# Kernel optimization log

Measured on AMD Instinct MI355X. Metric: run time of the kernel, lower is better.

The kernel has to match this reference:

```python
import jax, jax.numpy as jnp
import numpy as np

N = 100000        # nodes
E = 1600000       # edges
NFEAT = 256
NHID = 64
NCLASS = 40
NHEADS = 4
ALPHA = 0.2       # LeakyReLU negative slope


def setup_inputs() -> dict:
    key = jax.random.key(0)
    ks = jax.random.split(key, 7)
    h = jax.random.normal(ks[0], (N, NFEAT), jnp.float32)
    src = jax.random.randint(ks[1], (E,), 0, N, dtype=jnp.int32)
    dst = jax.random.randint(ks[2], (E,), 0, N, dtype=jnp.int32)
    edge_index = jnp.stack([src, dst])  # (2, E)
    # learned parameters (xavier-ish scale)
    W_heads = jax.random.normal(ks[3], (NHEADS, NFEAT, NHID), jnp.float32) * 0.066
    a_heads = jax.random.normal(ks[4], (NHEADS, 2 * NHID, 1), jnp.float32) * 0.1
    W_out = jax.random.normal(ks[5], (NHEADS * NHID, NCLASS), jnp.float32) * 0.08
    a_out = jax.random.normal(ks[6], (2 * NCLASS, 1), jnp.float32) * 0.1
    return {"h": h, "edge_index": edge_index, "W_heads": W_heads,
            "a_heads": a_heads, "W_out": W_out, "a_out": a_out}


def gat_layer(h, src, dst, W, a, concat):
    """One GraphAttentionLayer: gather -> per-edge score -> segment softmax -> scatter."""
    Wh = h @ W                                   # (n, F_out)
    n = h.shape[0]
    F_out = Wh.shape[1]
    # a_input @ a == Wh_src @ a[:F] + Wh_dst @ a[F:], avoids (E, 2F) concat
    a_src, a_dst = a[:F_out, 0], a[F_out:, 0]
    e = jax.nn.leaky_relu(Wh[src] @ a_src + Wh[dst] @ a_dst, ALPHA)  # (E,)
    # per-destination segment softmax (stabilized; same math as exp/sum)
    m = jax.ops.segment_max(e, dst, num_segments=n)
    exp_e = jnp.exp(e - m[dst])
    denom = jax.ops.segment_sum(exp_e, dst, num_segments=n)
    att = exp_e / denom[dst]                     # (E,)
    # scatter-aggregate weighted source features
    h_prime = jax.ops.segment_sum(att[:, None] * Wh[src], dst, num_segments=n)
    return jax.nn.elu(h_prime) if concat else h_prime


def reference(h, edge_index, W_heads, a_heads, W_out, a_out):
    src, dst = edge_index[0], edge_index[1]
    # multi-head attention layers, concatenated (dropout inactive in eval)
    x = jnp.concatenate(
        [gat_layer(h, src, dst, W_heads[i], a_heads[i], True) for i in range(NHEADS)],
        axis=1)                                  # (N, NHEADS*NHID)
    x = gat_layer(x, src, dst, W_out, a_out, False)  # (N, NCLASS)
    return jax.nn.log_softmax(x, axis=1)
```

## Files before the change

kernel.cpp:

```cpp
#include <hip/hip_runtime.h>


#define ALPHA 0.2f
constexpr int N_ = 100000;
constexpr int E_ = 1600000;
constexpr long OUTEL = (long)N_ * 40;

typedef __bf16 bf16x8 __attribute__((ext_vector_type(8)));
typedef float f32x4 __attribute__((ext_vector_type(4)));

__global__ void k_sent(float* out, long n, float v) {
    long i = blockIdx.x * 256L + threadIdx.x;
    if (i < n) out[i] = v;
}


__global__ void k_zero(int* p, int n) {
    int i = blockIdx.x * 256 + threadIdx.x;
    if (i < n) p[i] = 0;
}

__global__ void k_count(const int* __restrict__ dst, int* __restrict__ deg) {
    int e = blockIdx.x * 256 + threadIdx.x;
    if (e < E_) {
        int d = dst[e];
        if ((unsigned)d < (unsigned)N_) atomicAdd(&deg[d], 1);
    }
}

__global__ void k_partial(const int* __restrict__ deg, int* __restrict__ part) {
    __shared__ int sd[256];
    int b = blockIdx.x, t = threadIdx.x;
    int base = b * 1024;
    int s = 0;
    for (int i = 0; i < 4; i++) {
        int idx = base + t * 4 + i;
        if (idx < N_) s += deg[idx];
    }
    sd[t] = s;
    __syncthreads();
    for (int o = 128; o; o >>= 1) {
        if (t < o) sd[t] += sd[t + o];
        __syncthreads();
    }
    if (t == 0) part[b] = sd[0];
}

__global__ void k_scan_part(int* part, int nchunks, int* rowptr) {
    if (threadIdx.x == 0 && blockIdx.x == 0) {
        int run = 0;
        for (int b = 0; b < nchunks; b++) {
            int v = part[b];
            part[b] = run;
            run += v;
        }
        rowptr[N_] = run;
    }
}

__global__ void k_scan_final(const int* __restrict__ deg, const int* __restrict__ part,
                             int* __restrict__ rowptr, int* __restrict__ cursor) {
    __shared__ int sd[256];
    int b = blockIdx.x, t = threadIdx.x;
    int base = b * 1024;
    int v[4];
    int s = 0;
    for (int i = 0; i < 4; i++) {
        int idx = base + t * 4 + i;
        v[i] = (idx < N_) ? deg[idx] : 0;
        s += v[i];
    }
    sd[t] = s;
    __syncthreads();
    for (int o = 1; o < 256; o <<= 1) {
        int add = (t >= o) ? sd[t - o] : 0;
        __syncthreads();
        sd[t] += add;
        __syncthreads();
    }
    int off0 = part[b] + (sd[t] - s);
    for (int i = 0; i < 4; i++) {
        int idx = base + t * 4 + i;
        if (idx < N_) {
            rowptr[idx] = off0;
            cursor[idx] = off0;
            off0 += v[i];
        }
    }
}

__global__ void k_fill(const int* __restrict__ src, const int* __restrict__ dst,
                       int* __restrict__ cursor, int* __restrict__ csr) {
    int e = blockIdx.x * 256 + threadIdx.x;
    if (e < E_) {
        int d = dst[e];
        if ((unsigned)d < (unsigned)N_) {
            int p = atomicAdd(&cursor[d], 1);
            if ((unsigned)p < (unsigned)E_) csr[p] = src[e];
        }
    }
}


__global__ __launch_bounds__(320) void k_prepB(const float* __restrict__ Whd,
                                               const float* __restrict__ ah,
                                               __bf16* __restrict__ Bh, __bf16* __restrict__ Bl) {
    int k = blockIdx.x;
    int c = threadIdx.x;
    if (c >= 272) return;
    float v = 0.f;
    if (c < 256) {
        v = Whd[(c >> 6) * 16384 + k * 64 + (c & 63)];
    } else if (c < 264) {
        int hh = (c - 256) & 3;
        int isd = (c >= 260) ? 64 : 0;
        const float* wp = Whd + hh * 16384 + k * 64;
        const float* ap = ah + hh * 128 + isd;
        float s = 0.f;
        for (int j = 0; j < 64; j++) s += wp[j] * ap[j];
        v = s;
    }
    __bf16 hi = (__bf16)v;
    __bf16 lo = (__bf16)(v - (float)hi);
    size_t idx = ((size_t)(k >> 5) * 272 + c) * 32 + (k & 31);
    Bh[idx] = hi;
    Bl[idx] = lo;
}


__global__ __launch_bounds__(256) void k_gemm1m(const float* __restrict__ h,
                                                const __bf16* __restrict__ Bh,
                                                const __bf16* __restrict__ Bl,
                                                float* __restrict__ Wh1,
                                                float* __restrict__ s1s,
                                                float* __restrict__ s1d) {
    int t = threadIdx.x;
    int wv = t >> 6, l = t & 63;
    int l15 = l & 15, lg = l >> 4;
    int rowA = blockIdx.x * 64 + wv * 16 + l15;
    bool rok = rowA < N_;
    const float* hp = h + (size_t)rowA * 256 + lg * 8;

    f32x4 acc[17];
#pragma unroll
    for (int i = 0; i < 17; i++) acc[i] = (f32x4){0.f, 0.f, 0.f, 0.f};

    for (int kc = 0; kc < 8; kc++) {
        float va[8] = {0.f, 0.f, 0.f, 0.f, 0.f, 0.f, 0.f, 0.f};
        if (rok) {
            float4 p = *(const float4*)(hp + kc * 32);
            float4 q = *(const float4*)(hp + kc * 32 + 4);
            va[0] = p.x; va[1] = p.y; va[2] = p.z; va[3] = p.w;
            va[4] = q.x; va[5] = q.y; va[6] = q.z; va[7] = q.w;
        }
        bf16x8 ahi, alo;
#pragma unroll
        for (int j = 0; j < 8; j++) {
            __bf16 hi = (__bf16)va[j];
            ahi[j] = hi;
            alo[j] = (__bf16)(va[j] - (float)hi);
        }
        const __bf16* bph = Bh + ((size_t)kc * 272 + l15) * 32 + lg * 8;
        const __bf16* bpl = Bl + ((size_t)kc * 272 + l15) * 32 + lg * 8;
#pragma unroll
        for (int tt = 0; tt < 17; tt++) {
            bf16x8 bh = *(const bf16x8*)(bph + tt * 512);
            bf16x8 bl = *(const bf16x8*)(bpl + tt * 512);
            acc[tt] = __builtin_amdgcn_mfma_f32_16x16x32_bf16(ahi, bh, acc[tt], 0, 0, 0);
            acc[tt] = __builtin_amdgcn_mfma_f32_16x16x32_bf16(alo, bh, acc[tt], 0, 0, 0);
            acc[tt] = __builtin_amdgcn_mfma_f32_16x16x32_bf16(ahi, bl, acc[tt], 0, 0, 0);
        }
    }

    int rowD0 = blockIdx.x * 64 + wv * 16 + lg * 4;
#pragma unroll
    for (int tt = 0; tt < 16; tt++) {
#pragma unroll
        for (int r = 0; r < 4; r++) {
            int orow = rowD0 + r;
            if (orow < N_) Wh1[(size_t)orow * 256 + tt * 16 + l15] = acc[tt][r];
        }
    }
#pragma unroll
    for (int r = 0; r < 4; r++) {
        int orow = rowD0 + r;
        if (orow < N_) {
            if (l15 < 4) s1s[orow * 4 + l15] = acc[16][r];
            else if (l15 < 8) s1d[orow * 4 + (l15 - 4)] = acc[16][r];
        }
    }
}


__global__ __launch_bounds__(256) void k_att1(const int* __restrict__ rowptr, const int* __restrict__ csr,
                                              const float* __restrict__ s1s, const float* __restrict__ s1d,
                                              float* __restrict__ att1) {
    int t = threadIdx.x;
    int wv = t >> 6, l = t & 63;
    int n = blockIdx.x * 4 + wv;
    int base = rowptr[n], deg = rowptr[n + 1] - base;
    int i = l >> 2, hh = l & 3;
    float sdw = s1d[n * 4 + hh];

    float mx = -INFINITY;
    for (int ib = 0; ib < deg; ib += 16) {
        int e = ib + i;
        if (e < deg) {
            int s = csr[base + e];
            float v = s1s[s * 4 + hh] + sdw;
            v = v > 0.f ? v : ALPHA * v;
            mx = fmaxf(mx, v);
        }
    }
    for (int o = 4; o < 64; o <<= 1) mx = fmaxf(mx, __shfl_xor(mx, o));
    float sm = 0.f;
    for (int ib = 0; ib < deg; ib += 16) {
        int e = ib + i;
        if (e < deg) {
            int s = csr[base + e];
            float v = s1s[s * 4 + hh] + sdw;
            v = v > 0.f ? v : ALPHA * v;
            sm += expf(v - mx);
        }
    }
    for (int o = 4; o < 64; o <<= 1) sm += __shfl_xor(sm, o);
    float inv = (deg > 0) ? 1.f / sm : 0.f;
    for (int ib = 0; ib < deg; ib += 16) {
        int e = ib + i;
        if (e < deg) {
            int s = csr[base + e];
            float v = s1s[s * 4 + hh] + sdw;
            v = v > 0.f ? v : ALPHA * v;
            att1[(size_t)(base + e) * 4 + hh] = expf(v - mx) * inv;
        }
    }
}


constexpr int AGG_BLOCKS = 768;
constexpr int NODES_PER_SWEEP = AGG_BLOCKS * 8;

__global__ __launch_bounds__(512) void k_agg1g(const int* __restrict__ rowptr, const int* __restrict__ csr,
                                               const float* __restrict__ att1, const float* __restrict__ Wh1,
                                               const float* __restrict__ Wo, const float* __restrict__ ao,
                                               float* __restrict__ Wh2,
                                               float* __restrict__ s2s, float* __restrict__ s2d) {
    __shared__ float WoS[256 * 40];
    __shared__ float xs[8][256];
    int t = threadIdx.x;
#pragma unroll
    for (int u = 0; u < 5; u++) {
        int idx = (u * 512 + t) * 4;
        *(float4*)(&WoS[idx]) = *(const float4*)(&Wo[idx]);
    }
    __syncthreads();

    int w = t >> 6, lane = t & 63;
    int f = lane << 2;
    int hw = lane >> 4;
    float a1 = (lane < 40) ? ao[lane] : 0.f;
    float a2 = (lane < 40) ? ao[40 + lane] : 0.f;

    for (int n = blockIdx.x * 8 + w; n < N_; n += NODES_PER_SWEEP) {
        int base = rowptr[n], deg = rowptr[n + 1] - base;

        float4 acc = make_float4(0.f, 0.f, 0.f, 0.f);
        int i = 0;
        for (; i + 3 < deg; i += 4) {
            int b0 = base + i;
            int s0 = csr[b0], s1 = csr[b0 + 1], s2 = csr[b0 + 2], s3 = csr[b0 + 3];
            float at0 = att1[(size_t)b0 * 4 + hw];
            float at1 = att1[(size_t)(b0 + 1) * 4 + hw];
            float at2 = att1[(size_t)(b0 + 2) * 4 + hw];
            float at3 = att1[(size_t)(b0 + 3) * 4 + hw];
            float4 v0 = *(const float4*)(Wh1 + (size_t)s0 * 256 + f);
            float4 v1 = *(const float4*)(Wh1 + (size_t)s1 * 256 + f);
            float4 v2 = *(const float4*)(Wh1 + (size_t)s2 * 256 + f);
            float4 v3 = *(const float4*)(Wh1 + (size_t)s3 * 256 + f);
            acc.x += at0 * v0.x + at1 * v1.x + at2 * v2.x + at3 * v3.x;
            acc.y += at0 * v0.y + at1 * v1.y + at2 * v2.y + at3 * v3.y;
            acc.z += at0 * v0.z + at1 * v1.z + at2 * v2.z + at3 * v3.z;
            acc.w += at0 * v0.w + at1 * v1.w + at2 * v2.w + at3 * v3.w;
        }
        for (; i < deg; i++) {
            int s0 = csr[base + i];
            float at0 = att1[(size_t)(base + i) * 4 + hw];
            float4 v0 = *(const float4*)(Wh1 + (size_t)s0 * 256 + f);
            acc.x += at0 * v0.x;
            acc.y += at0 * v0.y;
            acc.z += at0 * v0.z;
            acc.w += at0 * v0.w;
        }
        acc.x = acc.x > 0.f ? acc.x : (expf(acc.x) - 1.f);
        acc.y = acc.y > 0.f ? acc.y : (expf(acc.y) - 1.f);
        acc.z = acc.z > 0.f ? acc.z : (expf(acc.z) - 1.f);
        acc.w = acc.w > 0.f ? acc.w : (expf(acc.w) - 1.f);
        *(float4*)(&xs[w][f]) = acc;

        float o = 0.f;
        if (lane < 40) {
            for (int k = 0; k < 256; k += 4) {
                float4 xk = *(const float4*)(&xs[w][k]);
                o += xk.x * WoS[k * 40 + lane] + xk.y * WoS[(k + 1) * 40 + lane] +
                     xk.z * WoS[(k + 2) * 40 + lane] + xk.w * WoS[(k + 3) * 40 + lane];
            }
            Wh2[(size_t)n * 40 + lane] = o;
        }
        float r1 = o * a1, r2 = o * a2;
        for (int off = 32; off; off >>= 1) {
            r1 += __shfl_xor(r1, off);
            r2 += __shfl_xor(r2, off);
        }
        if (lane == 0) {
            s2s[n] = r1;
            s2d[n] = r2;
        }
    }
}


__global__ __launch_bounds__(256) void k_l2(const int* __restrict__ rowptr, const int* __restrict__ csr,
                                            const float* __restrict__ s2s, const float* __restrict__ s2d,
                                            const float* __restrict__ Wh2, float* __restrict__ out) {
    int t = threadIdx.x;
    int wv = t >> 6, lane = t & 63;
    int n = blockIdx.x * 4 + wv;
    int base = rowptr[n], deg = rowptr[n + 1] - base;
    float sdw = s2d[n];

    float mx = -INFINITY;
    for (int i = lane; i < deg; i += 64) {
        int s = csr[base + i];
        float e = s2s[s] + sdw;
        e = e > 0.f ? e : ALPHA * e;
        mx = fmaxf(mx, e);
    }
    for (int o = 32; o; o >>= 1) mx = fmaxf(mx, __shfl_xor(mx, o));

    float acc0 = 0.f, acc1 = 0.f, sm0 = 0.f, sm1 = 0.f;
    int i = 0;
    for (; i + 1 < deg; i += 2) {
        int s0 = csr[base + i], s1 = csr[base + i + 1];
        float e0 = s2s[s0] + sdw;
        float e1 = s2s[s1] + sdw;
        e0 = e0 > 0.f ? e0 : ALPHA * e0;
        e1 = e1 > 0.f ? e1 : ALPHA * e1;
        float a0 = expf(e0 - mx);
        float a1 = expf(e1 - mx);
        sm0 += a0; sm1 += a1;
        if (lane < 40) {
            acc0 += a0 * Wh2[(size_t)s0 * 40 + lane];
            acc1 += a1 * Wh2[(size_t)s1 * 40 + lane];
        }
    }
    if (i < deg) {
        int s0 = csr[base + i];
        float e0 = s2s[s0] + sdw;
        e0 = e0 > 0.f ? e0 : ALPHA * e0;
        float a0 = expf(e0 - mx);
        sm0 += a0;
        if (lane < 40) acc0 += a0 * Wh2[(size_t)s0 * 40 + lane];
    }
    float inv = (deg > 0) ? 1.f / (sm0 + sm1) : 0.f;
    float acc = (acc0 + acc1) * inv;

    float v = (lane < 40) ? acc : -INFINITY;
    float mv = v;
    for (int o = 32; o; o >>= 1) mv = fmaxf(mv, __shfl_xor(mv, o));
    float ex = (lane < 40) ? expf(acc - mv) : 0.f;
    float se = ex;
    for (int o = 32; o; o >>= 1) se += __shfl_xor(se, o);
    if (lane < 40) out[(size_t)n * 40 + lane] = acc - mv - logf(se);
}


extern "C" void kernel_launch(void* const* d_in, const int* in_sizes, int n_in,
                              void* d_out, int out_size, void* d_ws, size_t ws_size,
                              hipStream_t stream) {
    const float* h   = (const float*)d_in[0];
    const int*   ei  = (const int*)d_in[1];
    const float* Whd = (const float*)d_in[2];
    const float* ah  = (const float*)d_in[3];
    const float* Wo  = (const float*)d_in[4];
    const float* ao  = (const float*)d_in[5];
    float* out = (float*)d_out;

    const int* src = ei;
    const int* dst = ei + E_;
    const int nchunks = (N_ + 1023) / 1024;

    char* ws = (char*)d_ws;
    size_t off = 0;
    auto alloc = [&](size_t bytes) -> char* {
        size_t a = (off + 255) & ~(size_t)255;
        off = a + bytes;
        return ws + a;
    };
    int* rowptr = (int*)alloc((size_t)(N_ + 1) * 4);
    int* cursor = (int*)alloc((size_t)N_ * 4);
    int* deg    = (int*)alloc((size_t)N_ * 4);
    int* part   = (int*)alloc((size_t)(nchunks + 1) * 4);
    int* csr    = (int*)alloc((size_t)E_ * 4);
    float* s1s  = (float*)alloc((size_t)N_ * 4 * 4);
    float* s1d  = (float*)alloc((size_t)N_ * 4 * 4);
    float* Wh2  = (float*)alloc((size_t)N_ * 40 * 4);
    float* s2s  = (float*)alloc((size_t)N_ * 4);
    float* s2d  = (float*)alloc((size_t)N_ * 4);
    __bf16* Bh  = (__bf16*)alloc((size_t)8 * 272 * 32 * 2);
    __bf16* Bl  = (__bf16*)alloc((size_t)8 * 272 * 32 * 2);
    float* att1 = (float*)alloc((size_t)E_ * 4 * 4);
    float* Wh1  = (float*)alloc((size_t)N_ * 256 * 4);
    size_t need = off + 256;

    if (ws_size < need) {
        k_sent<<<(int)((OUTEL + 255) / 256), 256, 0, stream>>>(out, OUTEL, -2.0f);
        return;
    }

    k_prepB<<<256, 320, 0, stream>>>(Whd, ah, Bh, Bl);

    k_zero<<<(N_ + 255) / 256, 256, 0, stream>>>(deg, N_);
    k_count<<<(E_ + 255) / 256, 256, 0, stream>>>(dst, deg);
    k_partial<<<nchunks, 256, 0, stream>>>(deg, part);
    k_scan_part<<<1, 64, 0, stream>>>(part, nchunks, rowptr);
    k_scan_final<<<nchunks, 256, 0, stream>>>(deg, part, rowptr, cursor);
    k_fill<<<(E_ + 255) / 256, 256, 0, stream>>>(src, dst, cursor, csr);

    k_gemm1m<<<(N_ + 63) / 64, 256, 0, stream>>>(h, Bh, Bl, Wh1, s1s, s1d);
    k_att1<<<N_ / 4, 256, 0, stream>>>(rowptr, csr, s1s, s1d, att1);

    k_agg1g<<<AGG_BLOCKS, 512, 0, stream>>>(rowptr, csr, att1, Wh1, Wo, ao, Wh2, s2s, s2d);

    k_l2<<<N_ / 4, 256, 0, stream>>>(rowptr, csr, s2s, s2d, Wh2, out);
}
```

Baseline: 905.9 us.

## Defer softmax normalization, use readlane matvec, and retile layer-2 aggregation

The attention kernel now stores unnormalized exponentials plus a per-node inverse sum, removing its third pass that re-gathered scores and recomputed exp. The aggregation kernel applies the inverse sum after accumulation, replaces the shared-memory staging of the hidden vector with readlane broadcasts for the 256x40 projection, and raises block count and occupancy hints. The layer-2 kernel splits the wave into 8 edge groups by 8 column groups of 5 classes, so edges are processed in parallel instead of serially two at a time. The cost is an extra small buffer, more shuffle reductions, and heavier register use from the unrolled readlane loop.

```diff
diff --git a/kernel.cpp b/kernel.cpp
--- a/kernel.cpp
+++ b/kernel.cpp
@@ -194,7 +194,7 @@
 
 __global__ __launch_bounds__(256) void k_att1(const int* __restrict__ rowptr, const int* __restrict__ csr,
                                               const float* __restrict__ s1s, const float* __restrict__ s1d,
-                                              float* __restrict__ att1) {
+                                              float* __restrict__ att1, float* __restrict__ sinv1) {
     int t = threadIdx.x;
     int wv = t >> 6, l = t & 63;
     int n = blockIdx.x * 4 + wv;
@@ -220,33 +220,26 @@
             int s = csr[base + e];
             float v = s1s[s * 4 + hh] + sdw;
             v = v > 0.f ? v : ALPHA * v;
-            sm += expf(v - mx);
+            float ex = expf(v - mx);
+            att1[(size_t)(base + e) * 4 + hh] = ex;
+            sm += ex;
         }
     }
     for (int o = 4; o < 64; o <<= 1) sm += __shfl_xor(sm, o);
-    float inv = (deg > 0) ? 1.f / sm : 0.f;
-    for (int ib = 0; ib < deg; ib += 16) {
-        int e = ib + i;
-        if (e < deg) {
-            int s = csr[base + e];
-            float v = s1s[s * 4 + hh] + sdw;
-            v = v > 0.f ? v : ALPHA * v;
-            att1[(size_t)(base + e) * 4 + hh] = expf(v - mx) * inv;
-        }
-    }
-}
-
-
-constexpr int AGG_BLOCKS = 768;
+    if (l < 4) sinv1[n * 4 + hh] = (deg > 0) ? 1.f / sm : 0.f;
+}
+
+
+constexpr int AGG_BLOCKS = 1024;
 constexpr int NODES_PER_SWEEP = AGG_BLOCKS * 8;
 
-__global__ __launch_bounds__(512) void k_agg1g(const int* __restrict__ rowptr, const int* __restrict__ csr,
-                                               const float* __restrict__ att1, const float* __restrict__ Wh1,
-                                               const float* __restrict__ Wo, const float* __restrict__ ao,
-                                               float* __restrict__ Wh2,
-                                               float* __restrict__ s2s, float* __restrict__ s2d) {
+__global__ __launch_bounds__(512, 8) void k_agg1g(const int* __restrict__ rowptr, const int* __restrict__ csr,
+                                                  const float* __restrict__ att1, const float* __restrict__ sinv1,
+                                                  const float* __restrict__ Wh1,
+                                                  const float* __restrict__ Wo, const float* __restrict__ ao,
+                                                  float* __restrict__ Wh2,
+                                                  float* __restrict__ s2s, float* __restrict__ s2d) {
     __shared__ float WoS[256 * 40];
-    __shared__ float xs[8][256];
     int t = threadIdx.x;
 #pragma unroll
     for (int u = 0; u < 5; u++) {
@@ -258,6 +251,7 @@
     int w = t >> 6, lane = t & 63;
     int f = lane << 2;
     int hw = lane >> 4;
+    int lane40 = (lane < 40) ? lane : 0;
     float a1 = (lane < 40) ? ao[lane] : 0.f;
     float a2 = (lane < 40) ? ao[40 + lane] : 0.f;
 
@@ -291,21 +285,26 @@
             acc.z += at0 * v0.z;
             acc.w += at0 * v0.w;
         }
+        float inv = sinv1[n * 4 + hw];
+        acc.x *= inv; acc.y *= inv; acc.z *= inv; acc.w *= inv;
         acc.x = acc.x > 0.f ? acc.x : (expf(acc.x) - 1.f);
         acc.y = acc.y > 0.f ? acc.y : (expf(acc.y) - 1.f);
         acc.z = acc.z > 0.f ? acc.z : (expf(acc.z) - 1.f);
         acc.w = acc.w > 0.f ? acc.w : (expf(acc.w) - 1.f);
-        *(float4*)(&xs[w][f]) = acc;
 
         float o = 0.f;
-        if (lane < 40) {
-            for (int k = 0; k < 256; k += 4) {
-                float4 xk = *(const float4*)(&xs[w][k]);
-                o += xk.x * WoS[k * 40 + lane] + xk.y * WoS[(k + 1) * 40 + lane] +
-                     xk.z * WoS[(k + 2) * 40 + lane] + xk.w * WoS[(k + 3) * 40 + lane];
-            }
-            Wh2[(size_t)n * 40 + lane] = o;
-        }
+#pragma unroll
+        for (int j = 0; j < 64; j++) {
+            float x0 = __uint_as_float(__builtin_amdgcn_readlane(__float_as_uint(acc.x), j));
+            float x1 = __uint_as_float(__builtin_amdgcn_readlane(__float_as_uint(acc.y), j));
+            float x2 = __uint_as_float(__builtin_amdgcn_readlane(__float_as_uint(acc.z), j));
+            float x3 = __uint_as_float(__builtin_amdgcn_readlane(__float_as_uint(acc.w), j));
+            int k4 = j * 4;
+            o += x0 * WoS[k4 * 40 + lane40] + x1 * WoS[(k4 + 1) * 40 + lane40] +
+                 x2 * WoS[(k4 + 2) * 40 + lane40] + x3 * WoS[(k4 + 3) * 40 + lane40];
+        }
+        if (lane < 40) Wh2[(size_t)n * 40 + lane] = o;
+
         float r1 = o * a1, r2 = o * a2;
         for (int off = 32; off; off >>= 1) {
             r1 += __shfl_xor(r1, off);
@@ -337,40 +336,48 @@
     }
     for (int o = 32; o; o >>= 1) mx = fmaxf(mx, __shfl_xor(mx, o));
 
-    float acc0 = 0.f, acc1 = 0.f, sm0 = 0.f, sm1 = 0.f;
-    int i = 0;
-    for (; i + 1 < deg; i += 2) {
-        int s0 = csr[base + i], s1 = csr[base + i + 1];
-        float e0 = s2s[s0] + sdw;
-        float e1 = s2s[s1] + sdw;
-        e0 = e0 > 0.f ? e0 : ALPHA * e0;
-        e1 = e1 > 0.f ? e1 : ALPHA * e1;
-        float a0 = expf(e0 - mx);
-        float a1 = expf(e1 - mx);
-        sm0 += a0; sm1 += a1;
-        if (lane < 40) {
-            acc0 += a0 * Wh2[(size_t)s0 * 40 + lane];
-            acc1 += a1 * Wh2[(size_t)s1 * 40 + lane];
-        }
-    }
-    if (i < deg) {
-        int s0 = csr[base + i];
-        float e0 = s2s[s0] + sdw;
-        e0 = e0 > 0.f ? e0 : ALPHA * e0;
-        float a0 = expf(e0 - mx);
-        sm0 += a0;
-        if (lane < 40) acc0 += a0 * Wh2[(size_t)s0 * 40 + lane];
-    }
-    float inv = (deg > 0) ? 1.f / (sm0 + sm1) : 0.f;
-    float acc = (acc0 + acc1) * inv;
-
-    float v = (lane < 40) ? acc : -INFINITY;
-    float mv = v;
-    for (int o = 32; o; o >>= 1) mv = fmaxf(mv, __shfl_xor(mv, o));
-    float ex = (lane < 40) ? expf(acc - mv) : 0.f;
-    float se = ex;
-    for (int o = 32; o; o >>= 1) se += __shfl_xor(se, o);
-    if (lane < 40) out[(size_t)n * 40 + lane] = acc - mv - logf(se);
+    int e8 = lane >> 3, c8 = lane & 7;
+    int cb = c8 * 5;
+    float acc0 = 0.f, acc1 = 0.f, acc2 = 0.f, acc3 = 0.f, acc4 = 0.f;
+    float smp = 0.f;
+    for (int i = e8; i < deg; i += 8) {
+        int s = csr[base + i];
+        float e = s2s[s] + sdw;
+        e = e > 0.f ? e : ALPHA * e;
+        float a = expf(e - mx);
+        smp += a;
+        const float* wp = Wh2 + (size_t)s * 40 + cb;
+        acc0 += a * wp[0];
+        acc1 += a * wp[1];
+        acc2 += a * wp[2];
+        acc3 += a * wp[3];
+        acc4 += a * wp[4];
+    }
+    for (int o = 8; o < 64; o <<= 1) {
+        smp += __shfl_xor(smp, o);
+        acc0 += __shfl_xor(acc0, o);
+        acc1 += __shfl_xor(acc1, o);
+        acc2 += __shfl_xor(acc2, o);
+        acc3 += __shfl_xor(acc3, o);
+        acc4 += __shfl_xor(acc4, o);
+    }
+    float inv = (deg > 0) ? 1.f / smp : 0.f;
+    acc0 *= inv; acc1 *= inv; acc2 *= inv; acc3 *= inv; acc4 *= inv;
+
+    float mv = fmaxf(fmaxf(fmaxf(acc0, acc1), fmaxf(acc2, acc3)), acc4);
+    for (int o = 1; o < 8; o <<= 1) mv = fmaxf(mv, __shfl_xor(mv, o));
+    float se = expf(acc0 - mv) + expf(acc1 - mv) + expf(acc2 - mv) +
+               expf(acc3 - mv) + expf(acc4 - mv);
+    for (int o = 1; o < 8; o <<= 1) se += __shfl_xor(se, o);
+    float lse = logf(se);
+    if (e8 == 0) {
+        float* op = out + (size_t)n * 40 + cb;
+        op[0] = acc0 - mv - lse;
+        op[1] = acc1 - mv - lse;
+        op[2] = acc2 - mv - lse;
+        op[3] = acc3 - mv - lse;
+        op[4] = acc4 - mv - lse;
+    }
 }
 
 
@@ -403,6 +410,7 @@
     int* csr    = (int*)alloc((size_t)E_ * 4);
     float* s1s  = (float*)alloc((size_t)N_ * 4 * 4);
     float* s1d  = (float*)alloc((size_t)N_ * 4 * 4);
+    float* sinv1= (float*)alloc((size_t)N_ * 4 * 4);
     float* Wh2  = (float*)alloc((size_t)N_ * 40 * 4);
     float* s2s  = (float*)alloc((size_t)N_ * 4);
     float* s2d  = (float*)alloc((size_t)N_ * 4);
@@ -427,9 +435,9 @@
     k_fill<<<(E_ + 255) / 256, 256, 0, stream>>>(src, dst, cursor, csr);
 
     k_gemm1m<<<(N_ + 63) / 64, 256, 0, stream>>>(h, Bh, Bl, Wh1, s1s, s1d);
-    k_att1<<<N_ / 4, 256, 0, stream>>>(rowptr, csr, s1s, s1d, att1);
-
-    k_agg1g<<<AGG_BLOCKS, 512, 0, stream>>>(rowptr, csr, att1, Wh1, Wo, ao, Wh2, s2s, s2d);
+    k_att1<<<N_ / 4, 256, 0, stream>>>(rowptr, csr, s1s, s1d, att1, sinv1);
+
+    k_agg1g<<<AGG_BLOCKS, 512, 0, stream>>>(rowptr, csr, att1, sinv1, Wh1, Wo, ao, Wh2, s2s, s2d);
 
     k_l2<<<N_ / 4, 256, 0, stream>>>(rowptr, csr, s2s, s2d, Wh2, out);
 }
```

Measured after the change: 2.247 ms. 148% more time.
